# Kernel optimization log

Hardware: AMD Instinct MI355X
Metric: run time of the kernel (lower is better)

## Reference

```python
import jax, jax.numpy as jnp
import numpy as np
from jax import lax

B, T, N, NIN, NOUT = 16, 32, 512, 32, 16
STEEP_GJ, STEEP_FIRE, STEEP_IN = 10.0, 10.0, 5.0
INPUT_THRESH, LEAKY_SLOPE = 0.01, 0.01
EDGE_P = 0.05


def setup_inputs() -> dict:
    key = jax.random.key(0)
    ks = jax.random.split(key, 7)
    obs_sequence = jax.random.normal(ks[0], (B, T, NIN), dtype=jnp.float32)
    weights = jax.random.uniform(ks[1], (N, N), dtype=jnp.float32) * 5.0
    thresholds = jax.random.uniform(ks[2], (N,), dtype=jnp.float32) * 5.0
    decay = jax.random.uniform(ks[3], (N,), dtype=jnp.float32) * 0.5
    mask_ex = jax.random.bernoulli(ks[4], EDGE_P, (N, N)).astype(jnp.float32)
    mask_in = jax.random.bernoulli(ks[5], EDGE_P, (N, N)).astype(jnp.float32)
    mask_gj = jax.random.bernoulli(ks[6], EDGE_P, (N, N)).astype(jnp.float32)
    input_indices = jnp.arange(NIN, dtype=jnp.int32)
    output_indices = NIN + jnp.arange(NOUT, dtype=jnp.int32)
    return {"obs_sequence": obs_sequence, "weights": weights, "thresholds": thresholds,
            "decay": decay, "mask_ex": mask_ex, "mask_in": mask_in, "mask_gj": mask_gj,
            "input_indices": input_indices, "output_indices": output_indices}


def reference(obs_sequence, weights, thresholds, decay, mask_ex, mask_in, mask_gj,
              input_indices, output_indices):
    # obs_encoder and action_decoder are identity: obs values drive input neurons,
    # action = E-state of output neurons.
    W_pos = jax.nn.softplus(weights)            # [N,N] (dst, src)
    W_chem = W_pos * (mask_ex - mask_in)        # excitatory minus inhibitory
    W_gj = W_pos * mask_gj                      # gap junctions

    def step(carry, obs_t):
        E, O = carry                            # [B,N] each
        O_h = O.at[:, input_indices].set(obs_t)
        E_h = E.at[:, input_indices].set(obs_t)
        # chemical synapse current: [B,N] @ [N,N]^T
        I_chem = O_h @ W_chem.T
        # gap junction current via O(B,N,N) broadcast, as in original
        diff = O_h[:, None, :] - E_h[:, :, None]          # [B, dst, src]
        direction = jnp.tanh(STEEP_GJ * diff)
        I_gj = jnp.einsum('ds,bs,bds->bd', W_gj, O_h, direction)
        curr = jnp.clip(E_h + I_chem + I_gj, -10.0, 10.0)
        z = curr - thresholds
        O_new = jnp.where(z >= 0, z, LEAKY_SLOPE * z)      # leaky_relu
        firing_gate = jax.nn.sigmoid(STEEP_FIRE * z)
        decay_gate = jax.nn.sigmoid(STEEP_IN * (jnp.abs(E_h - curr) - INPUT_THRESH))
        E_nonfired = decay_gate * curr + (1.0 - decay_gate) * (E_h - decay)
        E_new = firing_gate * O_new + (1.0 - firing_gate) * E_nonfired
        O_new = O_new.at[:, input_indices].set(obs_t)
        E_new = E_new.at[:, input_indices].set(obs_t)
        action = E_new[:, output_indices]
        return (E_new, O_new), action

    b, n = obs_sequence.shape[0], weights.shape[0]
    E0 = jnp.zeros((b, n), dtype=obs_sequence.dtype)
    O0 = jnp.zeros((b, n), dtype=obs_sequence.dtype)
    (_, _), actions = lax.scan(step, (E0, O0), jnp.swapaxes(obs_sequence, 0, 1))
    return jnp.swapaxes(actions, 0, 1)                    # [B,T,NOUT]
```

## Files before the change

### kernel.cpp

```cpp
#include <hip/hip_runtime.h>

#define N_NEUR 512
#define B_SZ   16
#define T_STEPS 32
#define NIN    32
#define NOUT   16
#define CAPC   84
#define CAPG   52
#define MC     42
#define MG     26
#define MCP    21
#define MGP    13
#define LOG2E  1.4426950408889634f

__device__ __forceinline__ float rcp_fast(float x) {
#if __has_builtin(__builtin_amdgcn_rcpf)
    return __builtin_amdgcn_rcpf(x);
#else
    return 1.0f / x;
#endif
}
__device__ __forceinline__ float exp2_fast(float x) {
#if __has_builtin(__builtin_amdgcn_exp2f)
    return __builtin_amdgcn_exp2f(x);
#else
    return exp2f(x);
#endif
}

__global__ __launch_bounds__(64) void prep1_kernel(
    const float* __restrict__ W,
    const float* __restrict__ mex,
    const float* __restrict__ min_,
    const float* __restrict__ mgj,
    int* __restrict__ key_arr, int* __restrict__ ccA, int* __restrict__ cgA,
    int2* __restrict__ tmpC, int2* __restrict__ tmpG)
{
    const int row  = blockIdx.x;
    const int lane = threadIdx.x;
    const unsigned long long below = (1ull << lane) - 1ull;
    int bc = 0, bg = 0;
    for (int c0 = 0; c0 < N_NEUR; c0 += 64) {
        const int col = c0 + lane;
        const int off = row * N_NEUR + col;
        const float w  = W[off];
        const float sp = fmaxf(w, 0.0f) + log1pf(__expf(-fabsf(w)));
        const float dm = mex[off] - min_[off];
        bool a = (dm != 0.0f);
        unsigned long long m = __ballot(a);
        int idx = bc + __popcll(m & below);
        if (a && idx < CAPC)
            tmpC[row * CAPC + idx] = make_int2(col, __float_as_int(sp * dm));
        bc += __popcll(m);

        const float g = mgj[off];
        bool ag = (g != 0.0f);
        m = __ballot(ag);
        idx = bg + __popcll(m & below);
        if (ag && idx < CAPG)
            tmpG[row * CAPG + idx] = make_int2(col, __float_as_int(sp * g));
        bg += __popcll(m);
    }
    if (lane == 0) {
        int cc = min(bc, CAPC), cg = min(bg, CAPG);
        ccA[row] = cc; cgA[row] = cg; key_arr[row] = cc + cg;
    }
}

__global__ __launch_bounds__(64) void prep2_kernel(
    const int* __restrict__ key_arr, const int* __restrict__ ccA, const int* __restrict__ cgA,
    const int2* __restrict__ tmpC, const int2* __restrict__ tmpG,
    int* __restrict__ order,
    float* __restrict__ wCt, unsigned* __restrict__ cpCt,
    float* __restrict__ wGt, unsigned* __restrict__ cpGt)
{
    __shared__ int   cS[CAPC];  __shared__ float wS[CAPC];
    __shared__ int   cSg[CAPG]; __shared__ float wSg[CAPG];
    __shared__ int   keyS[MC];
    __shared__ int   scol[MC];  __shared__ float sw[MC];
    const int d    = blockIdx.x;
    const int lane = threadIdx.x;
    const int kd   = key_arr[d];
    int r = 0;
    for (int j = lane; j < N_NEUR; j += 64) {
        int kj = key_arr[j];
        r += (kj < kd) || (kj == kd && j < d);
    }
    #pragma unroll
    for (int i = 1; i < 64; i <<= 1) r += __shfl_xor(r, i);
    if (lane == 0) order[r] = d;

    const int wv = r >> 5;
    const int Lb = 2 * (r & 31);
    const int cc = ccA[d], cg = cgA[d];

    for (int k = lane; k < CAPC; k += 64) {
        int2 e = (k < cc) ? tmpC[d * CAPC + k] : make_int2(0, 0);
        cS[k] = e.x; wS[k] = __int_as_float(e.y);
    }
    for (int k = lane; k < CAPG; k += 64) {
        int2 e = (k < cg) ? tmpG[d * CAPG + k] : make_int2(0, 0);
        cSg[k] = e.x; wSg[k] = __int_as_float(e.y);
    }
    __syncthreads();

    #pragma unroll
    for (int task = 0; task < 4; ++task) {
        const int isG = task >> 1, h = task & 1;
        const int cnt = isG ? cg : cc;
        const int m   = (cnt + 1 - h) >> 1;
        const int M   = isG ? MG : MC;
        const int MP  = isG ? MGP : MCP;
        const int myL = Lb + h;

        int col = 0; float w = 0.0f; int key = 0;
        if (lane < m) {
            col = isG ? cSg[2 * lane + h] : cS[2 * lane + h];
            w   = isG ? wSg[2 * lane + h] : wS[2 * lane + h];
            key = ((col & 31) - myL) & 31;
            keyS[lane] = key;
        }
        __syncthreads();
        if (lane < m) {
            int rk = 0;
            for (int j = 0; j < m; ++j) {
                int kj = keyS[j];
                rk += (kj < key) || (kj == key && j < lane);
            }
            scol[rk] = col; sw[rk] = w;
        }
        __syncthreads();
        float*    wT = isG ? wGt  : wCt;
        unsigned* cT = isG ? cpGt : cpCt;
        if (lane < M)
            wT[(wv * M + lane) * 64 + myL] = (lane < m) ? sw[lane] : 0.0f;
        if (lane < MP) {
            unsigned c0 = (2 * lane     < m) ? ((unsigned)scol[2 * lane]     << 2) : 0u;
            unsigned c1 = (2 * lane + 1 < m) ? ((unsigned)scol[2 * lane + 1] << 2) : 0u;
            cT[(wv * MP + lane) * 64 + myL] = c0 | (c1 << 16);
        }
        __syncthreads();
    }
}

#define CHEM_K(k, A) {                                                      \
    unsigned pk = cpC[(k) >> 1];                                            \
    unsigned off = ((k) & 1) ? (pk >> 16) : (pk & 0xffffu);                 \
    A = fmaf(wC[k], *(const float*)((const char*)ObP + off), A); }

#define CHEM_C4(a) { CHEM_K(a, accA) CHEM_K((a)+1, accB) CHEM_K((a)+2, accA) CHEM_K((a)+3, accB) }

#define GJ_K(k, A) {                                                        \
    unsigned pk = cpG[(k) >> 1];                                            \
    unsigned off = ((k) & 1) ? (pk >> 16) : (pk & 0xffffu);                 \
    float Os = *(const float*)((const char*)ObP + off);                     \
    float f = fmaf(20.0f * LOG2E, Os, cE);                                  \
    float tnh = 1.0f - 2.0f * rcp_fast(1.0f + exp2_fast(f));                \
    A = fmaf(wG[k] * Os, tnh, A); }

#define GJ_C4(a) { GJ_K(a, accA) GJ_K((a)+1, accB) GJ_K((a)+2, accA) GJ_K((a)+3, accB) }

__global__ __launch_bounds__(1024, 1) void recur_kernel(
    const float* __restrict__ obs,
    const float* __restrict__ thr,
    const float* __restrict__ dec,
    const int* __restrict__ order, const int* __restrict__ ccA, const int* __restrict__ cgA,
    const float* __restrict__ wCt, const unsigned* __restrict__ cpCt,
    const float* __restrict__ wGt, const unsigned* __restrict__ cpGt,
    float* __restrict__ out)
{
    __shared__ float Ob[2][N_NEUR];
    __shared__ float Eb[2][N_NEUR];

    const int b    = blockIdx.x;
    const int tid  = threadIdx.x;
    const int h    = tid & 1;
    const int r    = tid >> 1;
    const int wv   = tid >> 6;
    const int lane = tid & 63;

    const int d = order[r];
    const int cc = ccA[d];
    const int cg = cgA[d];
    const float thr_d = thr[d];
    const float dec_d = dec[d];

    int ccw = cc, cgw = cg;
    #pragma unroll
    for (int i = 1; i < 64; i <<= 1) {
        ccw = max(ccw, __shfl_xor(ccw, i));
        cgw = max(cgw, __shfl_xor(cgw, i));
    }
    const int mCw = __builtin_amdgcn_readfirstlane((ccw + 1) >> 1);
    const int mGw = __builtin_amdgcn_readfirstlane((cgw + 1) >> 1);

    float wC[MC]; unsigned cpC[MCP];
    float wG[MG]; unsigned cpG[MGP];
    #pragma unroll
    for (int k = 0; k < MC; ++k)  wC[k]  = wCt[(wv * MC + k) * 64 + lane];
    #pragma unroll
    for (int k = 0; k < MCP; ++k) cpC[k] = cpCt[(wv * MCP + k) * 64 + lane];
    #pragma unroll
    for (int k = 0; k < MG; ++k)  wG[k]  = wGt[(wv * MG + k) * 64 + lane];
    #pragma unroll
    for (int k = 0; k < MGP; ++k) cpG[k] = cpGt[(wv * MGP + k) * 64 + lane];

    const bool inj = (h == 0) && (d < NIN);
    const bool wr  = (h == 0) && (d >= NIN) && (d < NIN + NOUT);
    float* outp = out + (size_t)b * T_STEPS * NOUT + (d - NIN);
    const float* obs_b = obs + b * (T_STEPS * NIN);

    if (h == 0) {
        float v = (d < NIN) ? obs_b[d] : 0.0f;
        Ob[0][d] = v;
        Eb[0][d] = v;
    }
    int p = 0;
    __syncthreads();

    for (int t = 0; t < T_STEPS; ++t) {
        float ob_next = (inj && (t + 1 < T_STEPS)) ? obs_b[(t + 1) * NIN + d] : 0.0f;

        const float* ObP = Ob[p];
        const float E_d = Eb[p][d];
        float accA = 0.0f, accB = 0.0f;
        CHEM_C4(0)
        if ( 4 < mCw) CHEM_C4(4)
        if ( 8 < mCw) CHEM_C4(8)
        if (12 < mCw) CHEM_C4(12)
        if (16 < mCw) CHEM_C4(16)
        if (20 < mCw) CHEM_C4(20)
        if (24 < mCw) CHEM_C4(24)
        if (28 < mCw) CHEM_C4(28)
        if (32 < mCw) CHEM_C4(32)
        if (36 < mCw) CHEM_C4(36)
        if (40 < mCw) { CHEM_K(40, accA) CHEM_K(41, accB) }
        const float cE = -20.0f * LOG2E * E_d;
        GJ_C4(0)
        if ( 4 < mGw) GJ_C4(4)
        if ( 8 < mGw) GJ_C4(8)
        if (12 < mGw) GJ_C4(12)
        if (16 < mGw) GJ_C4(16)
        if (20 < mGw) GJ_C4(20)
        if (24 < mGw) { GJ_K(24, accA) GJ_K(25, accB) }

        float acc = accA + accB;
        acc += __shfl_xor(acc, 1);

        float curr = fminf(fmaxf(E_d + acc, -10.0f), 10.0f);
        float z = curr - thr_d;
        float O_new = (z >= 0.0f) ? z : 0.01f * z;
        float fg = rcp_fast(1.0f + exp2_fast(-10.0f * LOG2E * z));
        float dg = rcp_fast(1.0f + exp2_fast(-5.0f * LOG2E * (fabsf(E_d - curr) - 0.01f)));
        float E_nf  = dg * curr + (1.0f - dg) * (E_d - dec_d);
        float E_new = fg * O_new + (1.0f - fg) * E_nf;

        const int q = p ^ 1;
        if (h == 0) {
            Eb[q][d] = inj ? ob_next : E_new;
            Ob[q][d] = inj ? ob_next : O_new;
            if (wr) outp[t * NOUT] = E_new;
        }
        __syncthreads();
        p = q;
    }
}

extern "C" void kernel_launch(void* const* d_in, const int* in_sizes, int n_in,
                              void* d_out, int out_size, void* d_ws, size_t ws_size,
                              hipStream_t stream)
{
    const float* obs  = (const float*)d_in[0];
    const float* W    = (const float*)d_in[1];
    const float* thr  = (const float*)d_in[2];
    const float* dec  = (const float*)d_in[3];
    const float* mex  = (const float*)d_in[4];
    const float* min_ = (const float*)d_in[5];
    const float* mgj  = (const float*)d_in[6];
    float* out = (float*)d_out;

    char* ws = (char*)d_ws;
    int*   key_arr = (int*)(ws);
    int*   ccA     = (int*)(ws + 2048);
    int*   cgA     = (int*)(ws + 4096);
    int*   order   = (int*)(ws + 6144);
    int2*  tmpC    = (int2*)(ws + 8192);
    int2*  tmpG    = (int2*)(ws + 8192 + 344064);
    float* wCt     = (float*)(ws + 565248);
    unsigned* cpCt = (unsigned*)(ws + 737280);
    float* wGt     = (float*)(ws + 823296);
    unsigned* cpGt = (unsigned*)(ws + 929792);

    prep1_kernel<<<N_NEUR, 64, 0, stream>>>(W, mex, min_, mgj,
                                            key_arr, ccA, cgA, tmpC, tmpG);
    prep2_kernel<<<N_NEUR, 64, 0, stream>>>(key_arr, ccA, cgA, tmpC, tmpG,
                                            order, wCt, cpCt, wGt, cpGt);
    recur_kernel<<<B_SZ, 1024, 0, stream>>>(obs, thr, dec,
                                            order, ccA, cgA,
                                            wCt, cpCt, wGt, cpGt, out);
}
```

Measured before the change: 186.4 us.

## Replicate O buffer into three bank-shifted copies to cut LDS bank conflicts

New measurement: 206.3 us. 1.11x slower.

```diff
diff --git a/kernel.cpp b/kernel.cpp
--- a/kernel.cpp
+++ b/kernel.cpp
@@ -11,6 +11,9 @@
 #define MG     26
 #define MCP    21
 #define MGP    13
+#define OB_C1  545
+#define OB_C2  1090
+#define OB_STRIDE 1632
 #define LOG2E  1.4426950408889634f
 
 __device__ __forceinline__ float rcp_fast(float x) {
@@ -25,6 +28,13 @@
     return __builtin_amdgcn_exp2f(x);
 #else
     return exp2f(x);
+#endif
+}
+__device__ __forceinline__ float pair_swap(float x) {
+#if __has_builtin(__builtin_amdgcn_mov_dpp)
+    return __int_as_float(__builtin_amdgcn_mov_dpp(__float_as_int(x), 0xB1, 0xF, 0xF, true));
+#else
+    return __shfl_xor(x, 1);
 #endif
 }
 
@@ -78,6 +88,9 @@
     __shared__ int   cSg[CAPG]; __shared__ float wSg[CAPG];
     __shared__ int   keyS[MC];
     __shared__ int   scol[MC];  __shared__ float sw[MC];
+    __shared__ int   seff[MC];  __shared__ int   srho[MC];
+    __shared__ int   scol2[MC]; __shared__ float sw2[MC]; __shared__ int srho2[MC];
+    __shared__ int   usg[32];
     const int d    = blockIdx.x;
     const int lane = threadIdx.x;
     const int kd   = key_arr[d];
@@ -120,6 +133,7 @@
             key = ((col & 31) - myL) & 31;
             keyS[lane] = key;
         }
+        if (lane < 32) usg[lane] = 0;
         __syncthreads();
         if (lane < m) {
             int rk = 0;
@@ -130,13 +144,50 @@
             scol[rk] = col; sw[rk] = w;
         }
         __syncthreads();
+        if (lane == 0) {
+            for (int j = 0; j < m; ++j) {
+                int c  = scol[j];
+                int kb = ((c & 31) - myL) & 31;
+                int e0 = kb, e1 = (kb + 1) & 31, e2 = (kb + 2) & 31;
+                int u0 = usg[e0], u1 = usg[e1], u2 = usg[e2];
+                int e, rho;
+                if      (u0 == 0)            { e = e0; rho = 0; }
+                else if (u1 == 0)            { e = e1; rho = 1; }
+                else if (u2 == 0)            { e = e2; rho = 2; }
+                else if (u0 <= u1 && u0 <= u2) { e = e0; rho = 0; }
+                else if (u1 <= u2)           { e = e1; rho = 1; }
+                else                         { e = e2; rho = 2; }
+                usg[e]++;
+                seff[j] = e; srho[j] = rho;
+            }
+        }
+        __syncthreads();
+        if (lane < m) {
+            int e = seff[lane];
+            int rk = 0;
+            for (int j = 0; j < m; ++j) {
+                int ej = seff[j];
+                rk += (ej < e) || (ej == e && j < lane);
+            }
+            scol2[rk] = scol[lane]; sw2[rk] = sw[lane]; srho2[rk] = srho[lane];
+        }
+        __syncthreads();
         float*    wT = isG ? wGt  : wCt;
         unsigned* cT = isG ? cpGt : cpCt;
         if (lane < M)
-            wT[(wv * M + lane) * 64 + myL] = (lane < m) ? sw[lane] : 0.0f;
+            wT[(wv * M + lane) * 64 + myL] = (lane < m) ? sw2[lane] : 0.0f;
         if (lane < MP) {
-            unsigned c0 = (2 * lane     < m) ? ((unsigned)scol[2 * lane]     << 2) : 0u;
-            unsigned c1 = (2 * lane + 1 < m) ? ((unsigned)scol[2 * lane + 1] << 2) : 0u;
+            unsigned c0 = 0u, c1 = 0u;
+            if (2 * lane < m) {
+                int rho = srho2[2 * lane];
+                int base = (rho == 0) ? 0 : ((rho == 1) ? OB_C1 : OB_C2);
+                c0 = (unsigned)((base + scol2[2 * lane]) << 2);
+            }
+            if (2 * lane + 1 < m) {
+                int rho = srho2[2 * lane + 1];
+                int base = (rho == 0) ? 0 : ((rho == 1) ? OB_C1 : OB_C2);
+                c1 = (unsigned)((base + scol2[2 * lane + 1]) << 2);
+            }
             cT[(wv * MP + lane) * 64 + myL] = c0 | (c1 << 16);
         }
         __syncthreads();
@@ -169,7 +220,7 @@
     const float* __restrict__ wGt, const unsigned* __restrict__ cpGt,
     float* __restrict__ out)
 {
-    __shared__ float Ob[2][N_NEUR];
+    __shared__ float Ob[2][OB_STRIDE];
     __shared__ float Eb[2][N_NEUR];
 
     const int b    = blockIdx.x;
@@ -212,7 +263,7 @@
 
     if (h == 0) {
         float v = (d < NIN) ? obs_b[d] : 0.0f;
-        Ob[0][d] = v;
+        Ob[0][d] = v; Ob[0][OB_C1 + d] = v; Ob[0][OB_C2 + d] = v;
         Eb[0][d] = v;
     }
     int p = 0;
@@ -245,7 +296,7 @@
         if (24 < mGw) { GJ_K(24, accA) GJ_K(25, accB) }
 
         float acc = accA + accB;
-        acc += __shfl_xor(acc, 1);
+        acc += pair_swap(acc);
 
         float curr = fminf(fmaxf(E_d + acc, -10.0f), 10.0f);
         float z = curr - thr_d;
@@ -257,8 +308,9 @@
 
         const int q = p ^ 1;
         if (h == 0) {
+            float Ov = inj ? ob_next : O_new;
             Eb[q][d] = inj ? ob_next : E_new;
-            Ob[q][d] = inj ? ob_next : O_new;
+            Ob[q][d] = Ov; Ob[q][OB_C1 + d] = Ov; Ob[q][OB_C2 + d] = Ov;
             if (wr) outp[t * NOUT] = E_new;
         }
         __syncthreads();
```
